# Optimization experiments

Measured on AMD Instinct MI355X. Metric: run time of the kernel, lower is better.

The kernel has to match this reference:

```python
import jax, jax.numpy as jnp
import numpy as np

N = 4_000_000   # number of sparse voxels
H = 128         # parent-grid extent per axis (input coords < 256 -> parents < 128)


def setup_inputs() -> dict:
    key = jax.random.key(0)
    # col 0 = batch index, cols 1:4 = integer xyz voxel coords in [0, 256)
    coords = jax.random.randint(key, (N, 4), 0, 256, dtype=jnp.int32)
    # spnn.Conv3d(1,1,k=2) kernel: (2^3, in=1, out=1), constant-init to 1.0
    kernel = jnp.ones((8, 1, 1), dtype=jnp.float32)
    return {"coords": coords, "kernel": kernel}


def _fog(coords, kernel):
    b = coords[:, 0].astype(jnp.int64)
    xyz = coords[:, 1:]
    # pos(): 3-bit occupancy code from LSBs of xyz, feat = 2^code
    bits = xyz & 1                                        # (N, 3)
    pos = bits[:, 0] + 2 * bits[:, 1] + 4 * bits[:, 2]    # (N,) in [0, 8)
    feats = (jnp.int32(1) << pos).astype(jnp.float32)     # (N,) values {1,...,128}

    # 2x2x2 stride-2 sparse conv with all-ones kernel == sum over the 8 children
    # of each parent voxel. The child's kernel-offset index is exactly `pos`.
    pxyz = (xyz >> 1).astype(jnp.int64)                   # parent coords
    pkey = ((b * H + pxyz[:, 0]) * H + pxyz[:, 1]) * H + pxyz[:, 2]

    ukeys, inv = jnp.unique(pkey, size=N, fill_value=-1, return_inverse=True)
    inv = inv.ravel()

    contrib = feats * kernel[pos, 0, 0]                   # all-ones kernel -> feats
    out_feats = jax.ops.segment_sum(contrib, inv, num_segments=N)  # (N,)

    # decode unique parent keys back to (batch, x, y, z); pad slots -> -1
    valid = ukeys >= 0
    k = jnp.where(valid, ukeys, 0)
    oz = k % H
    k = k // H
    oy = k % H
    k = k // H
    ox = k % H
    ob = k // H
    out_coords = jnp.stack([ob, ox, oy, oz], axis=-1).astype(jnp.int32)
    out_coords = jnp.where(valid[:, None], out_coords, jnp.int32(-1))
    return out_coords, out_feats


def reference(coords, kernel):
    return _fog(coords, kernel)
```

## Files before the change

### kernel.cpp

```cpp
#include <hip/hip_runtime.h>

#define NB_BITS     14
#define N_BUCKETS   (1 << NB_BITS)
#define LOCAL_BITS  15
#define LOCAL_WORDS (1 << (LOCAL_BITS - 5))
#define LKMASK      ((1u << LOCAL_BITS) - 1u)
#define KEYMASK     0x1FFFFFFFu
#define NBLK        256
#define N_PART      8
#define FE_CAP      384
#define WPB         4
#define EGRID       (N_BUCKETS / WPB)

__device__ __forceinline__ unsigned make_key(int4 c) {
    return ((((unsigned)c.x << 7) | (unsigned)(c.y >> 1)) << 7 | (unsigned)(c.z >> 1)) << 7
         | (unsigned)(c.w >> 1);
}

template<int NW>
__device__ inline void block_scan(unsigned v, unsigned* wsum, unsigned& excl, unsigned& total) {
    int t = threadIdx.x, ln = t & 63, wv = t >> 6;
    unsigned incl = v;
    #pragma unroll
    for (int off = 1; off < 64; off <<= 1) {
        unsigned y = __shfl_up(incl, off, 64);
        if (ln >= off) incl += y;
    }
    if (ln == 63) wsum[wv] = incl;
    __syncthreads();
    if (wv == 0) {
        unsigned s = (ln < NW) ? wsum[ln] : 0u;
        #pragma unroll
        for (int off = 1; off < NW; off <<= 1) {
            unsigned y = __shfl_up(s, off, 64);
            if (ln >= off) s += y;
        }
        if (ln < NW) wsum[ln] = s;
    }
    __syncthreads();
    excl = (wv ? wsum[wv - 1] : 0u) + incl - v;
    total = wsum[NW - 1];
}

__global__ void hist_pass(const int4* __restrict__ coords,
                          unsigned* __restrict__ hist,
                          unsigned* __restrict__ skeys, int n, int chunk) {
    __shared__ unsigned h[N_BUCKETS];
    int k = blockIdx.x, t = threadIdx.x;
    for (int i = t; i < N_BUCKETS; i += 1024) h[i] = 0u;
    __syncthreads();
    int s = k * chunk, e = min(n, s + chunk);
    for (int i = s + t; i < e; i += 1024) {
        int4 c = coords[i];
        unsigned key = make_key(c);
        unsigned pos = (unsigned)((c.y & 1) | ((c.z & 1) << 1) | ((c.w & 1) << 2));
        skeys[i] = (pos << 29) | key;
        atomicAdd(&h[key >> LOCAL_BITS], 1u);
    }
    __syncthreads();
    for (int i = t; i < N_BUCKETS; i += 1024) hist[k * N_BUCKETS + i] = h[i];
}

__global__ void offs_pass(const unsigned* __restrict__ hist,
                          unsigned* __restrict__ offs,
                          unsigned* __restrict__ total) {
    int b = blockIdx.x * blockDim.x + threadIdx.x;
    unsigned run = 0;
    #pragma unroll 1
    for (int g = 0; g < N_PART; ++g)
        for (int j = 0; j < NBLK / N_PART; ++j) {
            int k = j * N_PART + g;
            offs[k * N_BUCKETS + b] = run;
            run += hist[k * N_BUCKETS + b];
        }
    total[b] = run;
}

__global__ void scan16k(const unsigned* __restrict__ in, unsigned* __restrict__ out) {
    __shared__ unsigned wsum[16];
    int t = threadIdx.x;
    unsigned v[16], sum = 0;
    #pragma unroll
    for (int i = 0; i < 16; ++i) { v[i] = in[t * 16 + i]; sum += v[i]; }
    unsigned excl, tot;
    block_scan<16>(sum, wsum, excl, tot);
    unsigned run = excl;
    #pragma unroll
    for (int i = 0; i < 16; ++i) { out[t * 16 + i] = run; run += v[i]; }
    if (t == 1023) out[N_BUCKETS] = run;
}

__global__ void scatter_pass(const unsigned* __restrict__ skeys,
                             const unsigned* __restrict__ offs,
                             const unsigned* __restrict__ pbase,
                             unsigned* __restrict__ pairs, int n, int chunk) {
    __shared__ unsigned cur[N_BUCKETS];
    int k = blockIdx.x, t = threadIdx.x;
    for (int i = t; i < N_BUCKETS; i += 1024)
        cur[i] = pbase[i] + offs[k * N_BUCKETS + i];
    __syncthreads();
    int s = k * chunk, e = min(n, s + chunk);
    for (int i = s + t; i < e; i += 1024) {
        unsigned pk = skeys[i];
        unsigned b = (pk & KEYMASK) >> LOCAL_BITS;
        unsigned j = atomicAdd(&cur[b], 1u);
        pairs[j] = pk;
    }
}

__global__ void __launch_bounds__(256, 8)
count_w(const unsigned* __restrict__ pairs,
        const unsigned* __restrict__ pbase,
        unsigned* __restrict__ ucount) {
    __shared__ unsigned bm[WPB][LOCAL_WORDS];
    int t = threadIdx.x, ln = t & 63, wv = t >> 6;
    int b = blockIdx.x * WPB + wv;
    uint4* bm4 = (uint4*)bm[wv];
    uint4 z = make_uint4(0u, 0u, 0u, 0u);
    #pragma unroll
    for (int m = 0; m < 4; ++m) bm4[ln * 4 + m] = z;
    unsigned s = pbase[b], e = pbase[b + 1];
    for (unsigned i = s + ln; i < e; i += 64) {
        unsigned k = pairs[i] & LKMASK;
        atomicOr(&bm[wv][k >> 5], 1u << (k & 31u));
    }
    unsigned v = 0;
    #pragma unroll
    for (int m = 0; m < 4; ++m) {
        uint4 q = bm4[ln * 4 + m];
        v += __popc(q.x) + __popc(q.y) + __popc(q.z) + __popc(q.w);
    }
    #pragma unroll
    for (int off = 1; off < 64; off <<= 1) v += __shfl_xor(v, off, 64);
    if (ln == 0) ucount[b] = v;
}

__global__ void __launch_bounds__(256, 4)
emit_w(const unsigned* __restrict__ pairs,
       const unsigned* __restrict__ pbase,
       const unsigned* __restrict__ ubase,
       const float* __restrict__ kern,
       float4* __restrict__ out_coords,
       float* __restrict__ out_feats, int n) {
    __shared__ unsigned bm[WPB][LOCAL_WORDS];
    __shared__ unsigned pfx[WPB][LOCAL_WORDS];
    __shared__ float    fe[WPB][FE_CAP];
    int t = threadIdx.x, ln = t & 63, wv = t >> 6;
    int b = blockIdx.x * WPB + wv;
    uint4* bm4 = (uint4*)bm[wv];
    uint4* pfx4 = (uint4*)pfx[wv];
    uint4 z = make_uint4(0u, 0u, 0u, 0u);
    #pragma unroll
    for (int m = 0; m < 4; ++m) bm4[ln * 4 + m] = z;
    for (int i = ln; i < FE_CAP; i += 64) fe[wv][i] = 0.f;
    unsigned s = pbase[b], e = pbase[b + 1];
    for (unsigned i = s + ln; i < e; i += 64) {
        unsigned k = pairs[i] & LKMASK;
        atomicOr(&bm[wv][k >> 5], 1u << (k & 31u));
    }
    unsigned w[16];
    #pragma unroll
    for (int m = 0; m < 4; ++m) {
        uint4 q = bm4[ln * 4 + m];
        w[4 * m] = q.x; w[4 * m + 1] = q.y; w[4 * m + 2] = q.z; w[4 * m + 3] = q.w;
    }
    unsigned ssum = 0;
    #pragma unroll
    for (int m = 0; m < 16; ++m) ssum += __popc(w[m]);
    unsigned incl = ssum;
    #pragma unroll
    for (int off = 1; off < 64; off <<= 1) {
        unsigned y = __shfl_up(incl, off, 64);
        if (ln >= off) incl += y;
    }
    unsigned count = __shfl(incl, 63, 64);
    unsigned run = incl - ssum;
    unsigned pv[16];
    #pragma unroll
    for (int m = 0; m < 16; ++m) { pv[m] = run; run += __popc(w[m]); }
    #pragma unroll
    for (int m = 0; m < 4; ++m)
        pfx4[ln * 4 + m] = make_uint4(pv[4 * m], pv[4 * m + 1], pv[4 * m + 2], pv[4 * m + 3]);
    for (unsigned i = s + ln; i < e; i += 64) {
        unsigned pk = pairs[i];
        unsigned k = pk & LKMASK;
        unsigned pos = pk >> 29;
        unsigned lr = pfx[wv][k >> 5] + __popc(bm[wv][k >> 5] & ((1u << (k & 31u)) - 1u));
        atomicAdd(&fe[wv][lr], (float)(1 << pos) * kern[pos]);
    }
    unsigned base = ubase[b];
    unsigned bbits = (unsigned)b << LOCAL_BITS;
    #pragma unroll
    for (int m = 0; m < 16; ++m) {
        unsigned bits = w[m], r = pv[m];
        unsigned wi = (unsigned)(ln * 16 + m);
        while (bits) {
            int bit = __ffs(bits) - 1;
            bits &= bits - 1;
            unsigned key = bbits | (wi << 5) | (unsigned)bit;
            out_coords[base + r] = make_float4((float)(key >> 21),
                                               (float)((key >> 14) & 127u),
                                               (float)((key >> 7) & 127u),
                                               (float)(key & 127u));
            ++r;
        }
    }
    for (unsigned i = ln; i < count; i += 64)
        out_feats[base + i] = fe[wv][i];
    unsigned total = ubase[N_BUCKETS];
    for (unsigned r = total + (unsigned)(blockIdx.x * 256 + t); r < (unsigned)n; r += EGRID * 256u) {
        out_coords[r] = make_float4(-1.f, -1.f, -1.f, -1.f);
        out_feats[r] = 0.f;
    }
}

extern "C" void kernel_launch(void* const* d_in, const int* in_sizes, int n_in,
                              void* d_out, int out_size, void* d_ws, size_t ws_size,
                              hipStream_t stream) {
    const int4* coords = (const int4*)d_in[0];
    const float* kern  = (const float*)d_in[1];
    int N = in_sizes[0] / 4;

    float* out = (float*)d_out;
    float4* out_coords = (float4*)out;
    float* out_feats = out + (size_t)4 * N;

    unsigned* pairs = (unsigned*)d_ws;
    unsigned* skeys = pairs + (size_t)N;
    unsigned* hist  = skeys + (size_t)N;
    unsigned* offs  = hist + (size_t)NBLK * N_BUCKETS;
    unsigned* total = offs + (size_t)NBLK * N_BUCKETS;
    unsigned* pbase = total + N_BUCKETS;
    unsigned* ucount = pbase + (N_BUCKETS + 1);
    unsigned* ubase  = ucount + N_BUCKETS;

    int chunk = (N + NBLK - 1) / NBLK;
    hist_pass<<<NBLK, 1024, 0, stream>>>(coords, hist, skeys, N, chunk);
    offs_pass<<<N_BUCKETS / 256, 256, 0, stream>>>(hist, offs, total);
    scan16k<<<1, 1024, 0, stream>>>(total, pbase);
    scatter_pass<<<NBLK, 1024, 0, stream>>>(skeys, offs, pbase, pairs, N, chunk);
    count_w<<<EGRID, 256, 0, stream>>>(pairs, pbase, ucount);
    scan16k<<<1, 1024, 0, stream>>>(ucount, ubase);
    emit_w<<<EGRID, 256, 0, stream>>>(pairs, pbase, ubase, kern, out_coords, out_feats, N);
}
```

Measured before the change: 238.7 us.

## Fuse front passes into one cooperative kernel and pack histograms to 16-bit

Merges the histogram, offsets, bucket scan, scatter, unique-count and count scan stages into a single cooperative kernel that uses grid.sync between phases, replacing six launches with one. Per-block histogram and offset counters are packed two per 32-bit word, halving their shared and global footprint. The emit kernel now writes output coordinates directly per input element using the computed rank, so duplicate children store the same value repeatedly, instead of walking the bitmap. Its prefix array is narrowed to 16-bit. The cost is grid-wide barriers across only 256 blocks, the risk of 16-bit counter overflow, and redundant coordinate stores.

```diff
diff --git a/kernel.cpp b/kernel.cpp
--- a/kernel.cpp
+++ b/kernel.cpp
@@ -1,24 +1,24 @@
 #include <hip/hip_runtime.h>
+#include <hip/hip_cooperative_groups.h>
+namespace cg = cooperative_groups;
 
 #define NB_BITS     14
 #define N_BUCKETS   (1 << NB_BITS)
 #define LOCAL_BITS  15
-#define LOCAL_WORDS (1 << (LOCAL_BITS - 5))
+#define LOCAL_WORDS 1024
 #define LKMASK      ((1u << LOCAL_BITS) - 1u)
 #define KEYMASK     0x1FFFFFFFu
 #define NBLK        256
 #define N_PART      8
 #define FE_CAP      384
-#define WPB         4
-#define EGRID       (N_BUCKETS / WPB)
+#define EGRID       (N_BUCKETS / 4)
 
 __device__ __forceinline__ unsigned make_key(int4 c) {
     return ((((unsigned)c.x << 7) | (unsigned)(c.y >> 1)) << 7 | (unsigned)(c.z >> 1)) << 7
          | (unsigned)(c.w >> 1);
 }
 
-template<int NW>
-__device__ inline void block_scan(unsigned v, unsigned* wsum, unsigned& excl, unsigned& total) {
+__device__ inline void block_scan16(unsigned v, unsigned* wsum, unsigned& excl, unsigned& total) {
     int t = threadIdx.x, ln = t & 63, wv = t >> 6;
     unsigned incl = v;
     #pragma unroll
@@ -29,186 +29,179 @@
     if (ln == 63) wsum[wv] = incl;
     __syncthreads();
     if (wv == 0) {
-        unsigned s = (ln < NW) ? wsum[ln] : 0u;
+        unsigned s = (ln < 16) ? wsum[ln] : 0u;
         #pragma unroll
-        for (int off = 1; off < NW; off <<= 1) {
+        for (int off = 1; off < 16; off <<= 1) {
             unsigned y = __shfl_up(s, off, 64);
             if (ln >= off) s += y;
         }
-        if (ln < NW) wsum[ln] = s;
+        if (ln < 16) wsum[ln] = s;
     }
     __syncthreads();
     excl = (wv ? wsum[wv - 1] : 0u) + incl - v;
-    total = wsum[NW - 1];
-}
-
-__global__ void hist_pass(const int4* __restrict__ coords,
-                          unsigned* __restrict__ hist,
-                          unsigned* __restrict__ skeys, int n, int chunk) {
-    __shared__ unsigned h[N_BUCKETS];
-    int k = blockIdx.x, t = threadIdx.x;
-    for (int i = t; i < N_BUCKETS; i += 1024) h[i] = 0u;
-    __syncthreads();
+    total = wsum[15];
+}
+
+__device__ inline void scan16k_dev(const unsigned* in, unsigned* out, unsigned* wsum) {
+    int t = threadIdx.x;
+    unsigned v[16], sum = 0;
+    #pragma unroll
+    for (int i = 0; i < 16; ++i) { v[i] = in[t * 16 + i]; sum += v[i]; }
+    unsigned excl, tot;
+    block_scan16(sum, wsum, excl, tot);
+    unsigned run = excl;
+    #pragma unroll
+    for (int i = 0; i < 16; ++i) { out[t * 16 + i] = run; run += v[i]; }
+    if (t == 1023) out[N_BUCKETS] = run;
+}
+
+__global__ void __launch_bounds__(1024, 4)
+fog_front(const int4* __restrict__ coords,
+          unsigned* __restrict__ skeys,
+          unsigned* __restrict__ pairs,
+          unsigned* __restrict__ hist32,
+          unsigned* __restrict__ offs32,
+          unsigned* __restrict__ total,
+          unsigned* __restrict__ pbase,
+          unsigned* __restrict__ ucount,
+          unsigned* __restrict__ ubase,
+          int n, int chunk) {
+    __shared__ unsigned buf[16384];
+    cg::grid_group grid = cg::this_grid();
+    int t = threadIdx.x, k = blockIdx.x;
     int s = k * chunk, e = min(n, s + chunk);
+
+    for (int i = t; i < 8192; i += 1024) buf[i] = 0u;
+    __syncthreads();
     for (int i = s + t; i < e; i += 1024) {
         int4 c = coords[i];
         unsigned key = make_key(c);
         unsigned pos = (unsigned)((c.y & 1) | ((c.z & 1) << 1) | ((c.w & 1) << 2));
         skeys[i] = (pos << 29) | key;
-        atomicAdd(&h[key >> LOCAL_BITS], 1u);
-    }
-    __syncthreads();
-    for (int i = t; i < N_BUCKETS; i += 1024) hist[k * N_BUCKETS + i] = h[i];
-}
-
-__global__ void offs_pass(const unsigned* __restrict__ hist,
-                          unsigned* __restrict__ offs,
-                          unsigned* __restrict__ total) {
-    int b = blockIdx.x * blockDim.x + threadIdx.x;
-    unsigned run = 0;
-    #pragma unroll 1
-    for (int g = 0; g < N_PART; ++g)
-        for (int j = 0; j < NBLK / N_PART; ++j) {
-            int k = j * N_PART + g;
-            offs[k * N_BUCKETS + b] = run;
-            run += hist[k * N_BUCKETS + b];
-        }
-    total[b] = run;
-}
-
-__global__ void scan16k(const unsigned* __restrict__ in, unsigned* __restrict__ out) {
-    __shared__ unsigned wsum[16];
-    int t = threadIdx.x;
-    unsigned v[16], sum = 0;
-    #pragma unroll
-    for (int i = 0; i < 16; ++i) { v[i] = in[t * 16 + i]; sum += v[i]; }
-    unsigned excl, tot;
-    block_scan<16>(sum, wsum, excl, tot);
-    unsigned run = excl;
-    #pragma unroll
-    for (int i = 0; i < 16; ++i) { out[t * 16 + i] = run; run += v[i]; }
-    if (t == 1023) out[N_BUCKETS] = run;
-}
-
-__global__ void scatter_pass(const unsigned* __restrict__ skeys,
-                             const unsigned* __restrict__ offs,
-                             const unsigned* __restrict__ pbase,
-                             unsigned* __restrict__ pairs, int n, int chunk) {
-    __shared__ unsigned cur[N_BUCKETS];
-    int k = blockIdx.x, t = threadIdx.x;
-    for (int i = t; i < N_BUCKETS; i += 1024)
-        cur[i] = pbase[i] + offs[k * N_BUCKETS + i];
-    __syncthreads();
-    int s = k * chunk, e = min(n, s + chunk);
+        unsigned b = key >> LOCAL_BITS;
+        atomicAdd(&buf[b >> 1], (b & 1) ? 65536u : 1u);
+    }
+    __syncthreads();
+    for (int i = t; i < 8192; i += 1024) hist32[k * 8192 + i] = buf[i];
+    grid.sync();
+
+    {
+        int gid = k * 1024 + t;
+        if (gid < 8192) {
+            unsigned r0 = 0, r1 = 0;
+            #pragma unroll 1
+            for (int g = 0; g < N_PART; ++g)
+                for (int j = 0; j < NBLK / N_PART; ++j) {
+                    int kk = j * N_PART + g;
+                    unsigned h = hist32[kk * 8192 + gid];
+                    offs32[kk * 8192 + gid] = r0 | (r1 << 16);
+                    r0 += h & 0xFFFFu; r1 += h >> 16;
+                }
+            total[2 * gid] = r0; total[2 * gid + 1] = r1;
+        }
+    }
+    grid.sync();
+
+    if (k == 0) scan16k_dev(total, pbase, buf);
+    grid.sync();
+
+    for (int i = t; i < N_BUCKETS; i += 1024) {
+        unsigned o = (offs32[k * 8192 + (i >> 1)] >> ((i & 1) * 16)) & 0xFFFFu;
+        buf[i] = pbase[i] + o;
+    }
+    __syncthreads();
     for (int i = s + t; i < e; i += 1024) {
         unsigned pk = skeys[i];
         unsigned b = (pk & KEYMASK) >> LOCAL_BITS;
-        unsigned j = atomicAdd(&cur[b], 1u);
+        unsigned j = atomicAdd(&buf[b], 1u);
         pairs[j] = pk;
     }
-}
-
-__global__ void __launch_bounds__(256, 8)
-count_w(const unsigned* __restrict__ pairs,
-        const unsigned* __restrict__ pbase,
-        unsigned* __restrict__ ucount) {
-    __shared__ unsigned bm[WPB][LOCAL_WORDS];
+    grid.sync();
+
+    {
+        int ln = t & 63, wv = t >> 6;
+        unsigned* bm = &buf[wv * LOCAL_WORDS];
+        int gw = k * 16 + wv;
+        #pragma unroll 1
+        for (int q = 0; q < 4; ++q) {
+            int b = gw * 4 + q;
+            #pragma unroll
+            for (int m = 0; m < 16; ++m) bm[64 * m + ln] = 0u;
+            unsigned ss = pbase[b], ee = pbase[b + 1];
+            for (unsigned i = ss + ln; i < ee; i += 64) {
+                unsigned lk = pairs[i] & LKMASK;
+                atomicOr(&bm[lk >> 5], 1u << (lk & 31u));
+            }
+            unsigned v = 0;
+            #pragma unroll
+            for (int m = 0; m < 16; ++m) v += __popc(bm[64 * m + ln]);
+            #pragma unroll
+            for (int off = 1; off < 64; off <<= 1) v += __shfl_xor(v, off, 64);
+            if (ln == 0) ucount[b] = v;
+        }
+    }
+    grid.sync();
+
+    if (k == 0) scan16k_dev(ucount, ubase, buf);
+}
+
+__global__ void __launch_bounds__(256, 5)
+emit_fin(const unsigned* __restrict__ pairs,
+         const unsigned* __restrict__ pbase,
+         const unsigned* __restrict__ ubase,
+         const float* __restrict__ kern,
+         float4* __restrict__ out_coords,
+         float* __restrict__ out_feats, int n) {
+    __shared__ unsigned       bmS[4][LOCAL_WORDS];
+    __shared__ unsigned short pfxS[4][LOCAL_WORDS];
+    __shared__ float          feS[4][FE_CAP];
     int t = threadIdx.x, ln = t & 63, wv = t >> 6;
-    int b = blockIdx.x * WPB + wv;
-    uint4* bm4 = (uint4*)bm[wv];
-    uint4 z = make_uint4(0u, 0u, 0u, 0u);
-    #pragma unroll
-    for (int m = 0; m < 4; ++m) bm4[ln * 4 + m] = z;
+    int b = blockIdx.x * 4 + wv;
+    unsigned* bm = bmS[wv];
+    unsigned short* pfx = pfxS[wv];
+    float* fe = feS[wv];
+    #pragma unroll
+    for (int m = 0; m < 16; ++m) bm[64 * m + ln] = 0u;
+    #pragma unroll
+    for (int i = ln; i < FE_CAP; i += 64) fe[i] = 0.f;
     unsigned s = pbase[b], e = pbase[b + 1];
     for (unsigned i = s + ln; i < e; i += 64) {
-        unsigned k = pairs[i] & LKMASK;
-        atomicOr(&bm[wv][k >> 5], 1u << (k & 31u));
-    }
-    unsigned v = 0;
-    #pragma unroll
-    for (int m = 0; m < 4; ++m) {
-        uint4 q = bm4[ln * 4 + m];
-        v += __popc(q.x) + __popc(q.y) + __popc(q.z) + __popc(q.w);
-    }
-    #pragma unroll
-    for (int off = 1; off < 64; off <<= 1) v += __shfl_xor(v, off, 64);
-    if (ln == 0) ucount[b] = v;
-}
-
-__global__ void __launch_bounds__(256, 4)
-emit_w(const unsigned* __restrict__ pairs,
-       const unsigned* __restrict__ pbase,
-       const unsigned* __restrict__ ubase,
-       const float* __restrict__ kern,
-       float4* __restrict__ out_coords,
-       float* __restrict__ out_feats, int n) {
-    __shared__ unsigned bm[WPB][LOCAL_WORDS];
-    __shared__ unsigned pfx[WPB][LOCAL_WORDS];
-    __shared__ float    fe[WPB][FE_CAP];
-    int t = threadIdx.x, ln = t & 63, wv = t >> 6;
-    int b = blockIdx.x * WPB + wv;
-    uint4* bm4 = (uint4*)bm[wv];
-    uint4* pfx4 = (uint4*)pfx[wv];
-    uint4 z = make_uint4(0u, 0u, 0u, 0u);
-    #pragma unroll
-    for (int m = 0; m < 4; ++m) bm4[ln * 4 + m] = z;
-    for (int i = ln; i < FE_CAP; i += 64) fe[wv][i] = 0.f;
-    unsigned s = pbase[b], e = pbase[b + 1];
-    for (unsigned i = s + ln; i < e; i += 64) {
-        unsigned k = pairs[i] & LKMASK;
-        atomicOr(&bm[wv][k >> 5], 1u << (k & 31u));
-    }
-    unsigned w[16];
-    #pragma unroll
-    for (int m = 0; m < 4; ++m) {
-        uint4 q = bm4[ln * 4 + m];
-        w[4 * m] = q.x; w[4 * m + 1] = q.y; w[4 * m + 2] = q.z; w[4 * m + 3] = q.w;
-    }
-    unsigned ssum = 0;
-    #pragma unroll
-    for (int m = 0; m < 16; ++m) ssum += __popc(w[m]);
-    unsigned incl = ssum;
-    #pragma unroll
-    for (int off = 1; off < 64; off <<= 1) {
-        unsigned y = __shfl_up(incl, off, 64);
-        if (ln >= off) incl += y;
-    }
-    unsigned count = __shfl(incl, 63, 64);
-    unsigned run = incl - ssum;
-    unsigned pv[16];
-    #pragma unroll
-    for (int m = 0; m < 16; ++m) { pv[m] = run; run += __popc(w[m]); }
-    #pragma unroll
-    for (int m = 0; m < 4; ++m)
-        pfx4[ln * 4 + m] = make_uint4(pv[4 * m], pv[4 * m + 1], pv[4 * m + 2], pv[4 * m + 3]);
+        unsigned lk = pairs[i] & LKMASK;
+        atomicOr(&bm[lk >> 5], 1u << (lk & 31u));
+    }
+    unsigned runbase = 0;
+    #pragma unroll
+    for (int m = 0; m < 16; ++m) {
+        unsigned wm = bm[64 * m + ln];
+        unsigned pc = __popc(wm);
+        unsigned incl = pc;
+        #pragma unroll
+        for (int off = 1; off < 64; off <<= 1) {
+            unsigned y = __shfl_up(incl, off, 64);
+            if (ln >= off) incl += y;
+        }
+        pfx[64 * m + ln] = (unsigned short)(runbase + incl - pc);
+        runbase += __shfl(incl, 63, 64);
+    }
+    unsigned count = runbase;
+    unsigned ub = ubase[b];
     for (unsigned i = s + ln; i < e; i += 64) {
         unsigned pk = pairs[i];
-        unsigned k = pk & LKMASK;
+        unsigned key = pk & KEYMASK;
         unsigned pos = pk >> 29;
-        unsigned lr = pfx[wv][k >> 5] + __popc(bm[wv][k >> 5] & ((1u << (k & 31u)) - 1u));
-        atomicAdd(&fe[wv][lr], (float)(1 << pos) * kern[pos]);
-    }
-    unsigned base = ubase[b];
-    unsigned bbits = (unsigned)b << LOCAL_BITS;
-    #pragma unroll
-    for (int m = 0; m < 16; ++m) {
-        unsigned bits = w[m], r = pv[m];
-        unsigned wi = (unsigned)(ln * 16 + m);
-        while (bits) {
-            int bit = __ffs(bits) - 1;
-            bits &= bits - 1;
-            unsigned key = bbits | (wi << 5) | (unsigned)bit;
-            out_coords[base + r] = make_float4((float)(key >> 21),
-                                               (float)((key >> 14) & 127u),
-                                               (float)((key >> 7) & 127u),
-                                               (float)(key & 127u));
-            ++r;
-        }
+        unsigned lk = key & LKMASK;
+        unsigned w = lk >> 5;
+        unsigned lr = (unsigned)pfx[w] + __popc(bm[w] & ((1u << (lk & 31u)) - 1u));
+        atomicAdd(&fe[lr], (float)(1u << pos) * kern[pos]);
+        out_coords[ub + lr] = make_float4((float)(key >> 21),
+                                          (float)((key >> 14) & 127u),
+                                          (float)((key >> 7) & 127u),
+                                          (float)(key & 127u));
     }
     for (unsigned i = ln; i < count; i += 64)
-        out_feats[base + i] = fe[wv][i];
-    unsigned total = ubase[N_BUCKETS];
-    for (unsigned r = total + (unsigned)(blockIdx.x * 256 + t); r < (unsigned)n; r += EGRID * 256u) {
+        out_feats[ub + i] = fe[i];
+    unsigned totalU = ubase[N_BUCKETS];
+    for (unsigned r = totalU + (unsigned)(blockIdx.x * 256 + t); r < (unsigned)n; r += EGRID * 256u) {
         out_coords[r] = make_float4(-1.f, -1.f, -1.f, -1.f);
         out_feats[r] = 0.f;
     }
@@ -225,21 +218,21 @@
     float4* out_coords = (float4*)out;
     float* out_feats = out + (size_t)4 * N;
 
-    unsigned* pairs = (unsigned*)d_ws;
-    unsigned* skeys = pairs + (size_t)N;
-    unsigned* hist  = skeys + (size_t)N;
-    unsigned* offs  = hist + (size_t)NBLK * N_BUCKETS;
-    unsigned* total = offs + (size_t)NBLK * N_BUCKETS;
-    unsigned* pbase = total + N_BUCKETS;
+    unsigned* pairs  = (unsigned*)d_ws;
+    unsigned* skeys  = pairs + (size_t)N;
+    unsigned* hist32 = skeys + (size_t)N;
+    unsigned* offs32 = hist32 + (size_t)NBLK * 8192;
+    unsigned* total  = offs32 + (size_t)NBLK * 8192;
+    unsigned* pbase  = total + N_BUCKETS;
     unsigned* ucount = pbase + (N_BUCKETS + 1);
     unsigned* ubase  = ucount + N_BUCKETS;
 
     int chunk = (N + NBLK - 1) / NBLK;
-    hist_pass<<<NBLK, 1024, 0, stream>>>(coords, hist, skeys, N, chunk);
-    offs_pass<<<N_BUCKETS / 256, 256, 0, stream>>>(hist, offs, total);
-    scan16k<<<1, 1024, 0, stream>>>(total, pbase);
-    scatter_pass<<<NBLK, 1024, 0, stream>>>(skeys, offs, pbase, pairs, N, chunk);
-    count_w<<<EGRID, 256, 0, stream>>>(pairs, pbase, ucount);
-    scan16k<<<1, 1024, 0, stream>>>(ucount, ubase);
-    emit_w<<<EGRID, 256, 0, stream>>>(pairs, pbase, ubase, kern, out_coords, out_feats, N);
-}
+    void* args[] = { (void*)&coords, (void*)&skeys, (void*)&pairs, (void*)&hist32,
+                     (void*)&offs32, (void*)&total, (void*)&pbase, (void*)&ucount,
+                     (void*)&ubase, (void*)&N, (void*)&chunk };
+    hipLaunchCooperativeKernel((const void*)fog_front, dim3(NBLK), dim3(1024),
+                               args, 0, stream);
+    emit_fin<<<EGRID, 256, 0, stream>>>(pairs, pbase, ubase, kern,
+                                        out_coords, out_feats, N);
+}
```

After: 439.2 us. +84.0%, slower.
